# Performance work log

Hardware: AMD Instinct MI355X
Metric: run time of the kernel (lower is better)

## Reference

```python
import jax, jax.numpy as jnp
import numpy as np

N_NODES = 100000
N_EDGES = 3200000


def gcn_conv(x, edge_index, W, b, num_nodes):
    # PyG GCNConv: linear transform, add self-loops, symmetric degree norm, scatter-add, bias
    h = x @ W  # [N, out]
    src = jnp.concatenate([edge_index[0], jnp.arange(num_nodes)])  # self-loops
    dst = jnp.concatenate([edge_index[1], jnp.arange(num_nodes)])
    deg = jax.ops.segment_sum(jnp.ones_like(dst, dtype=h.dtype), dst, num_segments=num_nodes)
    dinv = jnp.where(deg > 0, jax.lax.rsqrt(deg), 0.0)
    norm = dinv[src] * dinv[dst]  # [E+N]
    msg = h[src] * norm[:, None]  # gather + scale
    out = jax.ops.segment_sum(msg, dst, num_segments=num_nodes)  # scatter-add
    return out + b


def setup_inputs() -> dict:
    key = jax.random.key(0)
    k1, k2, k3, k4 = jax.random.split(key, 4)
    x = jax.random.normal(k1, (N_NODES, 18), dtype=jnp.float32)
    edge_index = jax.random.randint(k2, (2, N_EDGES), 0, N_NODES, dtype=jnp.int64)
    W1 = jax.random.normal(k3, (18, 64), dtype=jnp.float32) * (1.0 / np.sqrt(18))
    b1 = jnp.zeros((64,), dtype=jnp.float32)
    W2 = jax.random.normal(k4, (64, 32), dtype=jnp.float32) * (1.0 / np.sqrt(64))
    b2 = jnp.zeros((32,), dtype=jnp.float32)
    return {"x": x, "edge_index": edge_index, "W1": W1, "b1": b1, "W2": W2, "b2": b2}


def reference(x, edge_index, W1, b1, W2, b2):
    h = jax.nn.relu(gcn_conv(x, edge_index, W1, b1, N_NODES))
    return gcn_conv(h, edge_index, W2, b2, N_NODES)
```

## Files before the change

kernel.cpp:

```cpp
#include <hip/hip_runtime.h>
#include <hip/hip_fp16.h>

#define F0 18
#define F1 64
#define F2 32
#define BSHIFT 8
#define BNODES 256
#define CHUNK 8192
#define CAP 9216

__global__ __launch_bounds__(256) void scatter_sort_kernel(const int* __restrict__ ei,
                                                           int* __restrict__ bcur,
                                                           unsigned int* __restrict__ stage,
                                                           int E, int NB) {
    __shared__ unsigned int sbuf[CHUNK];
    __shared__ int lh[512];
    __shared__ int lofs[512];
    __shared__ int lb[512];
    __shared__ int tmp[256];
    int t = threadIdx.x;
    int e0 = blockIdx.x * CHUNK, e1 = min(e0 + CHUNK, E);
    int ec = e1 - e0;

    lh[t] = 0; lh[t + 256] = 0;
    __syncthreads();
    for (int e = e0 + t; e < e1; e += 256)
        atomicAdd(&lh[ei[E + e] >> BSHIFT], 1);
    __syncthreads();

    int c0 = lh[2 * t], c1 = lh[2 * t + 1];
    int s = c0 + c1;
    tmp[t] = s;
    __syncthreads();
    for (int off = 1; off < 256; off <<= 1) {
        int xv = (t >= off) ? tmp[t - off] : 0;
        __syncthreads();
        tmp[t] += xv;
        __syncthreads();
    }
    int ep = tmp[t] - s;
    lofs[2 * t] = ep;
    lofs[2 * t + 1] = ep + c0;
    if (2 * t < NB && c0 > 0) lb[2 * t] = 2 * t * CAP + atomicAdd(&bcur[2 * t], c0);
    if (2 * t + 1 < NB && c1 > 0) lb[2 * t + 1] = (2 * t + 1) * CAP + atomicAdd(&bcur[2 * t + 1], c1);
    lh[2 * t] = 0; lh[2 * t + 1] = 0;
    __syncthreads();

    for (int e = e0 + t; e < e1; e += 256) {
        int sN = ei[e], d = ei[E + e];
        int b = d >> BSHIFT;
        int pos = lofs[b] + atomicAdd(&lh[b], 1);
        sbuf[pos] = ((unsigned)(d & 255) << 24) | (unsigned)sN;
    }
    __syncthreads();

    int b;
    {
        int lo = 0, hi = NB;
        while (lo + 1 < hi) { int mid = (lo + hi) >> 1; if (lofs[mid] <= t) lo = mid; else hi = mid; }
        b = lo;
    }
    for (int i = t; i < ec; i += 256) {
        while (i >= lofs[b + 1]) ++b;
        int g = lb[b] + (i - lofs[b]);
        if (g < (b + 1) * CAP)
            stage[g] = sbuf[i];
    }
}

__global__ __launch_bounds__(256) void bucketfill_kernel(const unsigned int* __restrict__ stage,
                                                         const int* __restrict__ bcur,
                                                         int* __restrict__ rps,
                                                         int* __restrict__ rpe,
                                                         float* __restrict__ dinv,
                                                         int* __restrict__ csr,
                                                         const float* __restrict__ x,
                                                         __half* __restrict__ xp, int n) {
    __shared__ int lcnt[BNODES];
    __shared__ int lofs[BNODES];
    int b = blockIdx.x;
    int base = b << BSHIFT;
    int nn = min(BNODES, n - base);
    int ecnt = min(bcur[b], CAP);
    int estart = b * CAP;
    int t = threadIdx.x;

    lcnt[t] = 0;
    __syncthreads();
    for (int e = estart + t; e < estart + ecnt; e += 256)
        atomicAdd(&lcnt[stage[e] >> 24], 1);
    __syncthreads();

    int v = (t < nn) ? lcnt[t] : 0;
    lofs[t] = v;
    __syncthreads();
    for (int off = 1; off < BNODES; off <<= 1) {
        int xv = (t >= off) ? lofs[t - off] : 0;
        __syncthreads();
        lofs[t] += xv;
        __syncthreads();
    }
    float dv = rsqrtf((float)(v + 1));
    if (t < nn) {
        rps[base + t] = estart + lofs[t] - v;
        rpe[base + t] = estart + lofs[t];
        dinv[base + t] = dv;
    }
    __syncthreads();
    int cur0 = lofs[t] - v;
    __syncthreads();
    lcnt[t] = cur0;
    ((float*)lofs)[t] = dv;
    __syncthreads();

    for (int e = estart + t; e < estart + ecnt; e += 256) {
        unsigned int pk = stage[e];
        int d = pk >> 24;
        int pos = atomicAdd(&lcnt[d], 1);
        csr[estart + pos] = (int)(pk & 0xffffffu);
    }
    for (int idx = t; idx < nn * 32; idx += 256) {
        int lv = idx >> 5, j = idx & 31;
        float val = (j < F0) ? ((float*)lofs)[lv] * x[(size_t)(base + lv) * F0 + j] : 0.f;
        xp[(size_t)(base + lv) * 32 + j] = __float2half(val);
    }
}

struct __align__(8) h4v { __half2 a, b; };

__global__ __launch_bounds__(256) void agg32h_kernel(const __half* __restrict__ tab,
                                                     const int* __restrict__ csr,
                                                     const int* __restrict__ rps,
                                                     const int* __restrict__ rpe,
                                                     const float* __restrict__ dinv,
                                                     const float* __restrict__ bias,
                                                     float* __restrict__ outp, int n) {
    int wid = (blockIdx.x * 256 + threadIdx.x) >> 6;
    int lane = threadIdx.x & 63;
    if (wid >= n) return;
    int sub = lane >> 3;
    int q = (lane & 7) << 2;
    int beg = rps[wid], end = rpe[wid];
    float4 acc = make_float4(0.f, 0.f, 0.f, 0.f);
    if (sub == 0) {
        h4v sv = *(const h4v*)&tab[(size_t)wid * 32 + q];
        float2 f0 = __half22float2(sv.a), f1 = __half22float2(sv.b);
        acc.x = f0.x; acc.y = f0.y; acc.z = f1.x; acc.w = f1.y;
    }
    int e = beg + sub;
    for (; e + 8 < end; e += 16) {
        int s0 = csr[e], s1 = csr[e + 8];
        h4v v0 = *(const h4v*)&tab[(size_t)s0 * 32 + q];
        h4v v1 = *(const h4v*)&tab[(size_t)s1 * 32 + q];
        float2 a0 = __half22float2(v0.a), b0 = __half22float2(v0.b);
        float2 a1 = __half22float2(v1.a), b1 = __half22float2(v1.b);
        acc.x += a0.x + a1.x; acc.y += a0.y + a1.y;
        acc.z += b0.x + b1.x; acc.w += b0.y + b1.y;
    }
    for (; e < end; e += 8) {
        int s0 = csr[e];
        h4v v0 = *(const h4v*)&tab[(size_t)s0 * 32 + q];
        float2 a0 = __half22float2(v0.a), b0 = __half22float2(v0.b);
        acc.x += a0.x; acc.y += a0.y; acc.z += b0.x; acc.w += b0.y;
    }
    for (int off = 8; off < 64; off <<= 1) {
        acc.x += __shfl_xor(acc.x, off, 64);
        acc.y += __shfl_xor(acc.y, off, 64);
        acc.z += __shfl_xor(acc.z, off, 64);
        acc.w += __shfl_xor(acc.w, off, 64);
    }
    if (sub == 0) {
        float dv = dinv[wid];
        float4 r;
        r.x = acc.x * dv; r.y = acc.y * dv; r.z = acc.z * dv; r.w = acc.w * dv;
        if (bias) { r.x += bias[q]; r.y += bias[q + 1]; r.z += bias[q + 2]; r.w += bias[q + 3]; }
        *(float4*)&outp[(size_t)wid * 32 + q] = r;
    }
}

__global__ __launch_bounds__(256) void gemm_fused_kernel(const float* __restrict__ ax,
                                                         const float* __restrict__ W1,
                                                         const float* __restrict__ b1,
                                                         const float* __restrict__ W2,
                                                         const float* __restrict__ dinv,
                                                         __half* __restrict__ h2p, int n) {
    __shared__ float W1s[F0 * F1];
    __shared__ float W2s[F1 * F2];
    __shared__ float hid[8][F1];
    __shared__ float axs[8][32];
    int t = threadIdx.x;
    for (int i = t; i < F0 * F1; i += 256) W1s[i] = W1[i];
    for (int i = t; i < F1 * F2; i += 256) W2s[i] = W2[i];
    int lv = t >> 5, j = t & 31;
    int v = blockIdx.x * 8 + lv;
    if (v < n) axs[lv][j] = ax[(size_t)v * 32 + j];
    __syncthreads();
    float h0 = b1[j], h1 = b1[j + 32];
#pragma unroll
    for (int k = 0; k < F0; ++k) {
        float a = axs[lv][k];
        h0 += a * W1s[k * F1 + j];
        h1 += a * W1s[k * F1 + j + 32];
    }
    hid[lv][j] = fmaxf(h0, 0.f);
    hid[lv][j + 32] = fmaxf(h1, 0.f);
    __syncthreads();
    float acc = 0.f;
#pragma unroll
    for (int k = 0; k < F1; ++k) acc += hid[lv][k] * W2s[k * F2 + j];
    if (v < n) h2p[(size_t)v * 32 + j] = __float2half(acc * dinv[v]);
}


extern "C" void kernel_launch(void* const* d_in, const int* in_sizes, int n_in,
                              void* d_out, int out_size, void* d_ws, size_t ws_size,
                              hipStream_t stream) {
    const float* x  = (const float*)d_in[0];
    const int*   ei = (const int*)d_in[1];
    const float* W1 = (const float*)d_in[2];
    const float* b1 = (const float*)d_in[3];
    const float* W2 = (const float*)d_in[4];
    const float* b2 = (const float*)d_in[5];
    float* out = (float*)d_out;

    int n = in_sizes[0] / F0;
    int E = in_sizes[1] / 2;
    int NB = (n + BNODES - 1) >> BSHIFT;

    char* ws = (char*)d_ws;
    size_t o = 0;
    auto alloc = [&](size_t bytes) {
        char* p = ws + o;
        o = (o + bytes + 255) & ~(size_t)255;
        return p;
    };
    int*   rps   = (int*)alloc((size_t)n * 4);
    int*   rpe   = (int*)alloc((size_t)n * 4);
    float* dinv  = (float*)alloc((size_t)n * 4);
    int*   bcur  = (int*)alloc(512 * 4);
    int*   csr   = (int*)alloc((size_t)NB * CAP * 4);
    unsigned int* stage = (unsigned int*)alloc((size_t)NB * CAP * 4);
    float* ax    = (float*)alloc((size_t)n * 32 * 4);
    __half* xp   = (__half*)alloc((size_t)n * 32 * 2);
    __half* h2p  = (__half*)stage;
    (void)ws_size; (void)n_in; (void)out_size;

    int nchunks = (E + CHUNK - 1) / CHUNK;

    hipMemsetAsync(bcur, 0, 512 * 4, stream);
    scatter_sort_kernel<<<nchunks, 256, 0, stream>>>(ei, bcur, stage, E, NB);
    bucketfill_kernel<<<NB, 256, 0, stream>>>(stage, bcur, rps, rpe, dinv, csr, x, xp, n);

    agg32h_kernel<<<(n + 3) / 4, 256, 0, stream>>>(xp, csr, rps, rpe, dinv, nullptr, ax, n);
    gemm_fused_kernel<<<(n + 7) / 8, 256, 0, stream>>>(ax, W1, b1, W2, dinv, h2p, n);
    agg32h_kernel<<<(n + 3) / 4, 256, 0, stream>>>(h2p, csr, rps, rpe, dinv, b2, out, n);
}
```

Baseline: 242.5 us.

## Scatter edges directly to bucket staging without LDS local sort; widen bucketfill blocks

The scatter kernel drops its shared-memory local sort and prefix scan. Each edge now goes straight to its global bucket slot at a reserved offset plus a shared atomic counter. The chunk size shrinks so more blocks run with less shared memory each. The bucketfill kernel moves to 512 threads with a separate dinv array in shared memory. In exchange, global writes are less coalesced, and more blocks mean more global atomics on the bucket counters.

```diff
diff --git a/kernel.cpp b/kernel.cpp
--- a/kernel.cpp
+++ b/kernel.cpp
@@ -6,69 +6,38 @@
 #define F2 32
 #define BSHIFT 8
 #define BNODES 256
-#define CHUNK 8192
+#define CHUNK 2048
 #define CAP 9216
 
-__global__ __launch_bounds__(256) void scatter_sort_kernel(const int* __restrict__ ei,
-                                                           int* __restrict__ bcur,
-                                                           unsigned int* __restrict__ stage,
-                                                           int E, int NB) {
-    __shared__ unsigned int sbuf[CHUNK];
+__global__ __launch_bounds__(256) void scatter32_kernel(const int* __restrict__ ei,
+                                                        int* __restrict__ bcur,
+                                                        unsigned int* __restrict__ stage,
+                                                        int E, int NB) {
     __shared__ int lh[512];
-    __shared__ int lofs[512];
     __shared__ int lb[512];
-    __shared__ int tmp[256];
     int t = threadIdx.x;
+    for (int i = t; i < NB; i += 256) lh[i] = 0;
+    __syncthreads();
     int e0 = blockIdx.x * CHUNK, e1 = min(e0 + CHUNK, E);
-    int ec = e1 - e0;
-
-    lh[t] = 0; lh[t + 256] = 0;
-    __syncthreads();
     for (int e = e0 + t; e < e1; e += 256)
         atomicAdd(&lh[ei[E + e] >> BSHIFT], 1);
     __syncthreads();
-
-    int c0 = lh[2 * t], c1 = lh[2 * t + 1];
-    int s = c0 + c1;
-    tmp[t] = s;
-    __syncthreads();
-    for (int off = 1; off < 256; off <<= 1) {
-        int xv = (t >= off) ? tmp[t - off] : 0;
-        __syncthreads();
-        tmp[t] += xv;
-        __syncthreads();
-    }
-    int ep = tmp[t] - s;
-    lofs[2 * t] = ep;
-    lofs[2 * t + 1] = ep + c0;
-    if (2 * t < NB && c0 > 0) lb[2 * t] = 2 * t * CAP + atomicAdd(&bcur[2 * t], c0);
-    if (2 * t + 1 < NB && c1 > 0) lb[2 * t + 1] = (2 * t + 1) * CAP + atomicAdd(&bcur[2 * t + 1], c1);
-    lh[2 * t] = 0; lh[2 * t + 1] = 0;
-    __syncthreads();
-
+    for (int i = t; i < NB; i += 256) {
+        int c = lh[i];
+        lb[i] = c ? atomicAdd(&bcur[i], c) : 0;
+        lh[i] = 0;
+    }
+    __syncthreads();
     for (int e = e0 + t; e < e1; e += 256) {
-        int sN = ei[e], d = ei[E + e];
+        int s = ei[e], d = ei[E + e];
         int b = d >> BSHIFT;
-        int pos = lofs[b] + atomicAdd(&lh[b], 1);
-        sbuf[pos] = ((unsigned)(d & 255) << 24) | (unsigned)sN;
-    }
-    __syncthreads();
-
-    int b;
-    {
-        int lo = 0, hi = NB;
-        while (lo + 1 < hi) { int mid = (lo + hi) >> 1; if (lofs[mid] <= t) lo = mid; else hi = mid; }
-        b = lo;
-    }
-    for (int i = t; i < ec; i += 256) {
-        while (i >= lofs[b + 1]) ++b;
-        int g = lb[b] + (i - lofs[b]);
-        if (g < (b + 1) * CAP)
-            stage[g] = sbuf[i];
-    }
-}
-
-__global__ __launch_bounds__(256) void bucketfill_kernel(const unsigned int* __restrict__ stage,
+        int off = lb[b] + atomicAdd(&lh[b], 1);
+        if (off < CAP)
+            stage[(size_t)b * CAP + off] = ((unsigned)(d & 255) << 24) | (unsigned)s;
+    }
+}
+
+__global__ __launch_bounds__(512) void bucketfill_kernel(const unsigned int* __restrict__ stage,
                                                          const int* __restrict__ bcur,
                                                          int* __restrict__ rps,
                                                          int* __restrict__ rpe,
@@ -78,6 +47,7 @@
                                                          __half* __restrict__ xp, int n) {
     __shared__ int lcnt[BNODES];
     __shared__ int lofs[BNODES];
+    __shared__ float ldv[BNODES];
     int b = blockIdx.x;
     int base = b << BSHIFT;
     int nn = min(BNODES, n - base);
@@ -85,43 +55,42 @@
     int estart = b * CAP;
     int t = threadIdx.x;
 
-    lcnt[t] = 0;
-    __syncthreads();
-    for (int e = estart + t; e < estart + ecnt; e += 256)
+    if (t < BNODES) lcnt[t] = 0;
+    __syncthreads();
+    for (int e = estart + t; e < estart + ecnt; e += 512)
         atomicAdd(&lcnt[stage[e] >> 24], 1);
     __syncthreads();
 
-    int v = (t < nn) ? lcnt[t] : 0;
-    lofs[t] = v;
+    int v = 0;
+    if (t < BNODES) { v = (t < nn) ? lcnt[t] : 0; lofs[t] = v; }
     __syncthreads();
     for (int off = 1; off < BNODES; off <<= 1) {
-        int xv = (t >= off) ? lofs[t - off] : 0;
+        int xv = 0;
+        if (t < BNODES && t >= off) xv = lofs[t - off];
         __syncthreads();
-        lofs[t] += xv;
+        if (t < BNODES) lofs[t] += xv;
         __syncthreads();
     }
-    float dv = rsqrtf((float)(v + 1));
     if (t < nn) {
+        float dv = rsqrtf((float)(v + 1));
         rps[base + t] = estart + lofs[t] - v;
         rpe[base + t] = estart + lofs[t];
         dinv[base + t] = dv;
-    }
-    __syncthreads();
-    int cur0 = lofs[t] - v;
-    __syncthreads();
-    lcnt[t] = cur0;
-    ((float*)lofs)[t] = dv;
-    __syncthreads();
-
-    for (int e = estart + t; e < estart + ecnt; e += 256) {
+        ldv[t] = dv;
+    }
+    __syncthreads();
+    if (t < BNODES) lcnt[t] = lofs[t] - v;
+    __syncthreads();
+
+    for (int e = estart + t; e < estart + ecnt; e += 512) {
         unsigned int pk = stage[e];
         int d = pk >> 24;
         int pos = atomicAdd(&lcnt[d], 1);
         csr[estart + pos] = (int)(pk & 0xffffffu);
     }
-    for (int idx = t; idx < nn * 32; idx += 256) {
+    for (int idx = t; idx < nn * 32; idx += 512) {
         int lv = idx >> 5, j = idx & 31;
-        float val = (j < F0) ? ((float*)lofs)[lv] * x[(size_t)(base + lv) * F0 + j] : 0.f;
+        float val = (j < F0) ? ldv[lv] * x[(size_t)(base + lv) * F0 + j] : 0.f;
         xp[(size_t)(base + lv) * 32 + j] = __float2half(val);
     }
 }
@@ -248,8 +217,8 @@
     int nchunks = (E + CHUNK - 1) / CHUNK;
 
     hipMemsetAsync(bcur, 0, 512 * 4, stream);
-    scatter_sort_kernel<<<nchunks, 256, 0, stream>>>(ei, bcur, stage, E, NB);
-    bucketfill_kernel<<<NB, 256, 0, stream>>>(stage, bcur, rps, rpe, dinv, csr, x, xp, n);
+    scatter32_kernel<<<nchunks, 256, 0, stream>>>(ei, bcur, stage, E, NB);
+    bucketfill_kernel<<<NB, 512, 0, stream>>>(stage, bcur, rps, rpe, dinv, csr, x, xp, n);
 
     agg32h_kernel<<<(n + 3) / 4, 256, 0, stream>>>(xp, csr, rps, rpe, dinv, nullptr, ax, n);
     gemm_fused_kernel<<<(n + 7) / 8, 256, 0, stream>>>(ax, W1, b1, W2, dinv, h2p, n);
```

After: 250.8 us. 1.03x slower.
